# Performance work log

Hardware: AMD Instinct MI355X
Metric: run time of the kernel (lower is better)

Reference implementation:

```python
import jax, jax.numpy as jnp
import numpy as np

# Each of the 16 soft binary logic ops is a polynomial c0 + c1*a + c2*b + c3*a*b.
# Rows below are the [c0, c1, c2, c3] coefficients for ops 0..15 (same math as bin_op).
_OP_COEF = np.array([
    [0., 0., 0., 0.],   # 0: zeros
    [0., 0., 0., 1.],   # 1: a*b
    [0., 1., 0., -1.],  # 2: a - a*b
    [0., 1., 0., 0.],   # 3: a
    [0., 0., 1., -1.],  # 4: b - a*b
    [0., 0., 1., 0.],   # 5: b
    [0., 1., 1., -2.],  # 6: a + b - 2ab
    [0., 1., 1., -1.],  # 7: a + b - ab
    [1., -1., -1., 1.], # 8: 1 - (a + b - ab)
    [1., -1., -1., 2.], # 9: 1 - (a + b - 2ab)
    [1., 0., -1., 0.],  # 10: 1 - b
    [1., 0., -1., 1.],  # 11: 1 - b + ab
    [1., -1., 0., 0.],  # 12: 1 - a
    [1., -1., 0., 1.],  # 13: 1 - a + ab
    [1., 0., 0., -1.],  # 14: 1 - a*b
    [1., 0., 0., 0.],   # 15: ones
], dtype=np.float32)

K_CLASSES = 10
TAU = 30.0


def logic_layer(x, w, idx_a, idx_b):
    # x: [B, in_dim], w: [out_dim, 16], idx_a/idx_b: [out_dim]
    probs = jax.nn.softmax(w, axis=-1)                 # [O, 16]
    coef = probs @ jnp.asarray(_OP_COEF)               # [O, 4]
    a = x[:, idx_a]                                    # [B, O]
    b = x[:, idx_b]                                    # [B, O]
    # weighted mixture of 16 ops == polynomial in (1, a, b, a*b)
    return coef[:, 0] + coef[:, 1] * a + coef[:, 2] * b + coef[:, 3] * (a * b)


def group_sum(x, k, tau):
    B = x.shape[0]
    return x.reshape(B, k, x.shape[-1] // k).sum(-1) / tau


def setup_inputs() -> dict:
    key = jax.random.key(0)
    ks = jax.random.split(key, 10)
    B, D0, D1, D2, D3 = 4096, 1024, 8192, 8192, 10240
    return {
        "x": jax.random.uniform(ks[0], (B, D0), dtype=jnp.float32),
        "w1": jax.random.normal(ks[1], (D1, 16), dtype=jnp.float32),
        "w2": jax.random.normal(ks[2], (D2, 16), dtype=jnp.float32),
        "w3": jax.random.normal(ks[3], (D3, 16), dtype=jnp.float32),
        "idx_a1": jax.random.randint(ks[4], (D1,), 0, D0, dtype=jnp.int32),
        "idx_b1": jax.random.randint(ks[5], (D1,), 0, D0, dtype=jnp.int32),
        "idx_a2": jax.random.randint(ks[6], (D2,), 0, D1, dtype=jnp.int32),
        "idx_b2": jax.random.randint(ks[7], (D2,), 0, D1, dtype=jnp.int32),
        "idx_a3": jax.random.randint(ks[8], (D3,), 0, D2, dtype=jnp.int32),
        "idx_b3": jax.random.randint(ks[9], (D3,), 0, D2, dtype=jnp.int32),
    }


def reference(x, w1, w2, w3, idx_a1, idx_b1, idx_a2, idx_b2, idx_a3, idx_b3):
    h = logic_layer(x, w1, idx_a1, idx_b1)
    h = logic_layer(h, w2, idx_a2, idx_b2)
    h = logic_layer(h, w3, idx_a3, idx_b3)
    return group_sum(h, K_CLASSES, TAU)   # [B, 10]
```

## Files before the change

### kernel.cpp

```cpp
#include <hip/hip_runtime.h>
#include <hip/hip_fp16.h>
#include <stdint.h>

#define D0 1024
#define D1 8192
#define D2 8192
#define D3 10240
#define B_ROWS 4096

#define SM_XB     0
#define SM_H2     16384
#define SM_CSUM   (16384 + 131072)
#define SM_BYTES  (16384 + 131072 + 320)

__device__ __forceinline__ float4 softmax_coef(const float* __restrict__ w) {
    const float4* wv = (const float4*)w;
    float4 q0 = wv[0], q1 = wv[1], q2 = wv[2], q3 = wv[3];
    float wa[16] = {q0.x, q0.y, q0.z, q0.w, q1.x, q1.y, q1.z, q1.w,
                    q2.x, q2.y, q2.z, q2.w, q3.x, q3.y, q3.z, q3.w};
    float m = wa[0];
#pragma unroll
    for (int i = 1; i < 16; ++i) m = fmaxf(m, wa[i]);
    float e[16], s = 0.f;
#pragma unroll
    for (int i = 0; i < 16; ++i) { e[i] = __expf(wa[i] - m); s += e[i]; }
    float inv = 1.f / s;
    static constexpr float OPC[16][4] = {
        {0.f, 0.f, 0.f, 0.f}, {0.f, 0.f, 0.f, 1.f}, {0.f, 1.f, 0.f, -1.f}, {0.f, 1.f, 0.f, 0.f},
        {0.f, 0.f, 1.f, -1.f}, {0.f, 0.f, 1.f, 0.f}, {0.f, 1.f, 1.f, -2.f}, {0.f, 1.f, 1.f, -1.f},
        {1.f, -1.f, -1.f, 1.f}, {1.f, -1.f, -1.f, 2.f}, {1.f, 0.f, -1.f, 0.f}, {1.f, 0.f, -1.f, 1.f},
        {1.f, -1.f, 0.f, 0.f}, {1.f, -1.f, 0.f, 1.f}, {1.f, 0.f, 0.f, -1.f}, {1.f, 0.f, 0.f, 0.f}};
    float c0 = 0.f, c1 = 0.f, c2 = 0.f, c3 = 0.f;
#pragma unroll
    for (int i = 0; i < 16; ++i) {
        float p = e[i] * inv;
        c0 += p * OPC[i][0];
        c1 += p * OPC[i][1];
        c2 += p * OPC[i][2];
        c3 += p * OPC[i][3];
    }
    return make_float4(c0, c1, c2, c3);
}

__device__ __forceinline__ uint2 pack_coef(float4 c) {
    uint2 r;
    r.x = __builtin_bit_cast(uint32_t, __floats2half2_rn(c.x, c.y));
    r.y = __builtin_bit_cast(uint32_t, __floats2half2_rn(c.z, c.w));
    return r;
}

__global__ __launch_bounds__(64) void prep_kernel(
    const float* __restrict__ w1, const float* __restrict__ w2,
    const float* __restrict__ w3,
    const int* __restrict__ ia1, const int* __restrict__ ib1,
    const int* __restrict__ ia2, const int* __restrict__ ib2,
    const int* __restrict__ ia3, const int* __restrict__ ib3,
    uint4* __restrict__ bcM1, uint4* __restrict__ bcM2,
    uint4* __restrict__ d3M) {
    int G = blockIdx.x * 64 + threadIdx.x;
    if (G < D2) {
        int g = G;
        int pa = ia2[g], pb = ib2[g];
        float4 cO = softmax_coef(w2 + (size_t)g * 16);
        float4 cA = softmax_coef(w1 + (size_t)pa * 16);
        float4 cB = softmax_coef(w1 + (size_t)pb * 16);
        uint32_t xiA = (uint32_t)(ia1[pa] << 4) | ((uint32_t)(ib1[pa] << 4) << 16);
        uint32_t xiB = (uint32_t)(ia1[pb] << 4) | ((uint32_t)(ib1[pb] << 4) << 16);
        uint2 o = pack_coef(cO), a = pack_coef(cA), b = pack_coef(cB);
        bcM1[g] = make_uint4(xiA, xiB, o.x, o.y);
        bcM2[g] = make_uint4(a.x, a.y, b.x, b.y);
    } else {
        int g = G - D2;
        float4 cO = softmax_coef(w3 + (size_t)g * 16);
        uint2 o = pack_coef(cO);
        uint32_t ei = (uint32_t)ia3[g] | ((uint32_t)ib3[g] << 16);
        d3M[g] = make_uint4(ei, o.x, o.y, 0u);
    }
}

__device__ __forceinline__ uint4 gate8(uint4 av, uint4 bv, uint2 cf) {
    __half2 p = __builtin_bit_cast(__half2, cf.x);
    __half2 q = __builtin_bit_cast(__half2, cf.y);
    __half2 c0 = __low2half2(p), c1 = __high2half2(p);
    __half2 c2 = __low2half2(q), c3 = __high2half2(q);
    uint4 r;
#pragma unroll
    for (int i = 0; i < 4; ++i) {
        __half2 a = __builtin_bit_cast(__half2, (&av.x)[i]);
        __half2 b = __builtin_bit_cast(__half2, (&bv.x)[i]);
        __half2 h = __hfma2(a, __hfma2(b, c3, c1), __hfma2(b, c2, c0));
        (&r.x)[i] = __builtin_bit_cast(uint32_t, h);
    }
    return r;
}

__global__ __launch_bounds__(1024, 4) void fused_kernel(
    const float* __restrict__ x, const uint4* __restrict__ bcM1,
    const uint4* __restrict__ bcM2, const uint4* __restrict__ d3M,
    float* __restrict__ out) {
    extern __shared__ char sm[];
    uint4* xb = (uint4*)(sm + SM_XB);
    float* csum = (float*)(sm + SM_CSUM);

    const int t = threadIdx.x;
    const int rowbase = blockIdx.x << 3;
    const int tg = t << 1;

    uint4 m1a_n = bcM1[tg];
    uint4 m1b_n = bcM1[tg + 1];

    {
        const float* xp = x + (size_t)rowbase * D0 + t;
        uint4 v;
#pragma unroll
        for (int i = 0; i < 4; ++i) {
            float va = xp[(size_t)(2 * i) * D0];
            float vb = xp[(size_t)(2 * i + 1) * D0];
            (&v.x)[i] = __builtin_bit_cast(uint32_t, __floats2half2_rn(va, vb));
        }
        xb[t] = v;
    }
    if (t < 80) csum[t] = 0.f;
    __syncthreads();

#pragma unroll
    for (int k = 0; k < 4; ++k) {
        uint4 m1a = m1a_n, m1b = m1b_n;
        int g = tg + (k << 11);
        uint4 m2a = bcM2[g];
        uint4 m2b = bcM2[g + 1];
        if (k < 3) {
            int gn = tg + ((k + 1) << 11);
            m1a_n = bcM1[gn];
            m1b_n = bcM1[gn + 1];
        }
        uint4 aa0 = *(const uint4*)(sm + (m1a.x & 0xffffu));
        uint4 ab0 = *(const uint4*)(sm + (m1a.x >> 16));
        uint4 ba0 = *(const uint4*)(sm + (m1a.y & 0xffffu));
        uint4 bb0 = *(const uint4*)(sm + (m1a.y >> 16));
        uint4 aa1 = *(const uint4*)(sm + (m1b.x & 0xffffu));
        uint4 ab1 = *(const uint4*)(sm + (m1b.x >> 16));
        uint4 ba1 = *(const uint4*)(sm + (m1b.y & 0xffffu));
        uint4 bb1 = *(const uint4*)(sm + (m1b.y >> 16));
        uint4 h0 = gate8(gate8(aa0, ab0, make_uint2(m2a.x, m2a.y)),
                         gate8(ba0, bb0, make_uint2(m2a.z, m2a.w)),
                         make_uint2(m1a.z, m1a.w));
        uint4 h1v = gate8(gate8(aa1, ab1, make_uint2(m2b.x, m2b.y)),
                          gate8(ba1, bb1, make_uint2(m2b.z, m2b.w)),
                          make_uint2(m1b.z, m1b.w));
        *(uint4*)(sm + SM_H2 + ((uint32_t)g << 4)) = h0;
        *(uint4*)(sm + SM_H2 + ((uint32_t)(g + 1) << 4)) = h1v;
    }
    __syncthreads();

    {
        const int wv = t >> 6, lane = t & 63;
        const int gbase = wv * 640;
        const int cA = gbase >> 10;
        const int bnd = (cA + 1) << 10;
        float s0[8] = {0.f, 0.f, 0.f, 0.f, 0.f, 0.f, 0.f, 0.f};
        float s1[8] = {0.f, 0.f, 0.f, 0.f, 0.f, 0.f, 0.f, 0.f};
#pragma unroll
        for (int j = 0; j < 5; ++j) {
            int gc = gbase + (j << 7);
            int g = gc + (lane << 1);
            uint4 ma = d3M[g];
            uint4 mb = d3M[g + 1];
            uint4 av0 = *(const uint4*)(sm + SM_H2 + ((ma.x & 0xffffu) << 4));
            uint4 bv0 = *(const uint4*)(sm + SM_H2 + ((ma.x >> 16) << 4));
            uint4 av1 = *(const uint4*)(sm + SM_H2 + ((mb.x & 0xffffu) << 4));
            uint4 bv1 = *(const uint4*)(sm + SM_H2 + ((mb.x >> 16) << 4));
            uint4 h0 = gate8(av0, bv0, make_uint2(ma.y, ma.z));
            uint4 h1v = gate8(av1, bv1, make_uint2(mb.y, mb.z));
            float* s = (gc < bnd) ? s0 : s1;
#pragma unroll
            for (int i = 0; i < 4; ++i) {
                __half2 pr = __hadd2(__builtin_bit_cast(__half2, (&h0.x)[i]),
                                     __builtin_bit_cast(__half2, (&h1v.x)[i]));
                s[2 * i] += __low2float(pr);
                s[2 * i + 1] += __high2float(pr);
            }
        }
#pragma unroll
        for (int m = 1; m < 64; m <<= 1) {
#pragma unroll
            for (int r = 0; r < 8; ++r) {
                s0[r] += __shfl_xor(s0[r], m, 64);
                s1[r] += __shfl_xor(s1[r], m, 64);
            }
        }
        if (lane == 0) {
#pragma unroll
            for (int r = 0; r < 8; ++r) atomicAdd(&csum[cA * 8 + r], s0[r]);
            if (gbase + 640 > bnd) {
#pragma unroll
                for (int r = 0; r < 8; ++r) atomicAdd(&csum[(cA + 1) * 8 + r], s1[r]);
            }
        }
    }
    __syncthreads();

    if (t < 80) {
        int c = t >> 3, r = t & 7;
        out[(size_t)(rowbase + r) * 10 + c] = csum[t] * (1.0f / 30.0f);
    }
}

extern "C" void kernel_launch(void* const* d_in, const int* in_sizes, int n_in,
                              void* d_out, int out_size, void* d_ws, size_t ws_size,
                              hipStream_t stream) {
    const float* x = (const float*)d_in[0];
    const float* w1 = (const float*)d_in[1];
    const float* w2 = (const float*)d_in[2];
    const float* w3 = (const float*)d_in[3];
    const int* ia1 = (const int*)d_in[4];
    const int* ib1 = (const int*)d_in[5];
    const int* ia2 = (const int*)d_in[6];
    const int* ib2 = (const int*)d_in[7];
    const int* ia3 = (const int*)d_in[8];
    const int* ib3 = (const int*)d_in[9];
    float* out = (float*)d_out;

    char* p = (char*)d_ws;
    uint4* bcM1 = (uint4*)p;    p += (size_t)D2 * 16;
    uint4* bcM2 = (uint4*)p;    p += (size_t)D2 * 16;
    uint4* d3M = (uint4*)p;

    hipFuncSetAttribute(reinterpret_cast<const void*>(fused_kernel),
                        hipFuncAttributeMaxDynamicSharedMemorySize, SM_BYTES);

    prep_kernel<<<(D2 + D3) / 64, 64, 0, stream>>>(
        w1, w2, w3, ia1, ib1, ia2, ib2, ia3, ib3, bcM1, bcM2, d3M);
    fused_kernel<<<B_ROWS / 8, 1024, SM_BYTES, stream>>>(x, bcM1, bcM2, d3M, out);
}
```

Before: 106.5 us.

## Split prep work across more threads and use DPP wave reductions

The prep kernel now gives the layer-1 coefficient softmaxes for the A and B parents their own threads, uses 256-thread blocks and launches roughly twice as many threads, so the per-thread serial softmax chain is shorter. In the fused kernel, the 64-wide shuffle-xor butterfly reduction is replaced by a DPP row-shift and row-broadcast reduction that leaves the total in lane 63. The second partial-sum reduction is skipped for waves whose range does not cross a class boundary. The aim is to cut prep-kernel latency and the cost of the cross-lane reduction, at the price of extra redundant index loads in prep and hand-written DPP control codes.

After: 99.78 us. 1.07x faster.

```diff
diff --git a/kernel.cpp b/kernel.cpp
--- a/kernel.cpp
+++ b/kernel.cpp
@@ -49,7 +49,8 @@
     return r;
 }
 
-__global__ __launch_bounds__(64) void prep_kernel(
+#define PREP_TOTAL (3 * D2 + D3)
+__global__ __launch_bounds__(256) void prep_kernel(
     const float* __restrict__ w1, const float* __restrict__ w2,
     const float* __restrict__ w3,
     const int* __restrict__ ia1, const int* __restrict__ ib1,
@@ -57,20 +58,27 @@
     const int* __restrict__ ia3, const int* __restrict__ ib3,
     uint4* __restrict__ bcM1, uint4* __restrict__ bcM2,
     uint4* __restrict__ d3M) {
-    int G = blockIdx.x * 64 + threadIdx.x;
+    int G = blockIdx.x * 256 + threadIdx.x;
     if (G < D2) {
         int g = G;
         int pa = ia2[g], pb = ib2[g];
         float4 cO = softmax_coef(w2 + (size_t)g * 16);
-        float4 cA = softmax_coef(w1 + (size_t)pa * 16);
-        float4 cB = softmax_coef(w1 + (size_t)pb * 16);
         uint32_t xiA = (uint32_t)(ia1[pa] << 4) | ((uint32_t)(ib1[pa] << 4) << 16);
         uint32_t xiB = (uint32_t)(ia1[pb] << 4) | ((uint32_t)(ib1[pb] << 4) << 16);
-        uint2 o = pack_coef(cO), a = pack_coef(cA), b = pack_coef(cB);
+        uint2 o = pack_coef(cO);
         bcM1[g] = make_uint4(xiA, xiB, o.x, o.y);
-        bcM2[g] = make_uint4(a.x, a.y, b.x, b.y);
+    } else if (G < 2 * D2) {
+        int g = G - D2;
+        int pa = ia2[g];
+        uint2 a = pack_coef(softmax_coef(w1 + (size_t)pa * 16));
+        ((uint2*)bcM2)[2 * g] = a;
+    } else if (G < 3 * D2) {
+        int g = G - 2 * D2;
+        int pb = ib2[g];
+        uint2 b = pack_coef(softmax_coef(w1 + (size_t)pb * 16));
+        ((uint2*)bcM2)[2 * g + 1] = b;
     } else {
-        int g = G - D2;
+        int g = G - 3 * D2;
         float4 cO = softmax_coef(w3 + (size_t)g * 16);
         uint2 o = pack_coef(cO);
         uint32_t ei = (uint32_t)ia3[g] | ((uint32_t)ib3[g] << 16);
@@ -92,6 +100,20 @@
         (&r.x)[i] = __builtin_bit_cast(uint32_t, h);
     }
     return r;
+}
+
+__device__ __forceinline__ float dpp_sum_f32(float x) {
+#define DPPADD(ctrl, rmask)                                              \
+    x += __builtin_bit_cast(float, __builtin_amdgcn_update_dpp(          \
+             0, __builtin_bit_cast(int, x), (ctrl), (rmask), 0xf, true))
+    DPPADD(0x111, 0xf);
+    DPPADD(0x112, 0xf);
+    DPPADD(0x114, 0xf);
+    DPPADD(0x118, 0xf);
+    DPPADD(0x142, 0xa);
+    DPPADD(0x143, 0xc);
+#undef DPPADD
+    return x;
 }
 
 __global__ __launch_bounds__(1024, 4) void fused_kernel(
@@ -158,6 +180,7 @@
         const int gbase = wv * 640;
         const int cA = gbase >> 10;
         const int bnd = (cA + 1) << 10;
+        const bool cross = (gbase + 640 > bnd);
         float s0[8] = {0.f, 0.f, 0.f, 0.f, 0.f, 0.f, 0.f, 0.f};
         float s1[8] = {0.f, 0.f, 0.f, 0.f, 0.f, 0.f, 0.f, 0.f};
 #pragma unroll
@@ -172,27 +195,32 @@
             uint4 bv1 = *(const uint4*)(sm + SM_H2 + ((mb.x >> 16) << 4));
             uint4 h0 = gate8(av0, bv0, make_uint2(ma.y, ma.z));
             uint4 h1v = gate8(av1, bv1, make_uint2(mb.y, mb.z));
-            float* s = (gc < bnd) ? s0 : s1;
+            float pr8[8];
 #pragma unroll
             for (int i = 0; i < 4; ++i) {
                 __half2 pr = __hadd2(__builtin_bit_cast(__half2, (&h0.x)[i]),
                                      __builtin_bit_cast(__half2, (&h1v.x)[i]));
-                s[2 * i] += __low2float(pr);
-                s[2 * i + 1] += __high2float(pr);
+                pr8[2 * i] = __low2float(pr);
+                pr8[2 * i + 1] = __high2float(pr);
             }
-        }
-#pragma unroll
-        for (int m = 1; m < 64; m <<= 1) {
-#pragma unroll
-            for (int r = 0; r < 8; ++r) {
-                s0[r] += __shfl_xor(s0[r], m, 64);
-                s1[r] += __shfl_xor(s1[r], m, 64);
+            if (gc < bnd) {
+#pragma unroll
+                for (int r = 0; r < 8; ++r) s0[r] += pr8[r];
+            } else {
+#pragma unroll
+                for (int r = 0; r < 8; ++r) s1[r] += pr8[r];
             }
         }
-        if (lane == 0) {
+#pragma unroll
+        for (int r = 0; r < 8; ++r) s0[r] = dpp_sum_f32(s0[r]);
+        if (cross) {
+#pragma unroll
+            for (int r = 0; r < 8; ++r) s1[r] = dpp_sum_f32(s1[r]);
+        }
+        if (lane == 63) {
 #pragma unroll
             for (int r = 0; r < 8; ++r) atomicAdd(&csum[cA * 8 + r], s0[r]);
-            if (gbase + 640 > bnd) {
+            if (cross) {
 #pragma unroll
                 for (int r = 0; r < 8; ++r) atomicAdd(&csum[(cA + 1) * 8 + r], s1[r]);
             }
@@ -229,7 +257,7 @@
     hipFuncSetAttribute(reinterpret_cast<const void*>(fused_kernel),
                         hipFuncAttributeMaxDynamicSharedMemorySize, SM_BYTES);
 
-    prep_kernel<<<(D2 + D3) / 64, 64, 0, stream>>>(
+    prep_kernel<<<PREP_TOTAL / 256, 256, 0, stream>>>(
         w1, w2, w3, ia1, ib1, ia2, ib2, ia3, ib3, bcM1, bcM2, d3M);
     fused_kernel<<<B_ROWS / 8, 1024, SM_BYTES, stream>>>(x, bcM1, bcM2, d3M, out);
 }
```
